# Optimization experiments

Hardware: AMD Instinct MI355X
Metric: run time of the kernel (lower is better)

## Reference

```python
import jax, jax.numpy as jnp
import numpy as np

B, S, D, H = 4, 2048, 1024, 16
HD = D // H


def setup_inputs() -> dict:
    key = jax.random.key(0)
    ks = jax.random.split(key, 12)
    sc = 0.02
    inp = {
        "q": jax.random.normal(ks[0], (B, S, D), jnp.float32),
        "k": jax.random.normal(ks[1], (B, S, D), jnp.float32),
        "v": jax.random.normal(ks[2], (B, S, D), jnp.float32),
        "mask": jnp.tril(jnp.ones((S, S), jnp.int32))[None, None],  # causal [1,1,S,S]
        "Wq": jax.random.normal(ks[3], (D, D), jnp.float32) * sc,
        "bq": jnp.zeros((D,), jnp.float32),
        "Wk": jax.random.normal(ks[4], (D, D), jnp.float32) * sc,
        "bk": jnp.zeros((D,), jnp.float32),
        "Wv": jax.random.normal(ks[5], (D, D), jnp.float32) * sc,
        "bv": jnp.zeros((D,), jnp.float32),
        "Wo": jax.random.normal(ks[6], (D, D), jnp.float32) * sc,
        "bo": jnp.zeros((D,), jnp.float32),
    }
    return inp


def reference(q, k, v, mask, Wq, bq, Wk, bk, Wv, bv, Wo, bo):
    # Linear projections (torch Linear: x @ W.T + b)
    qh = (q @ Wq.T + bq).reshape(B, S, H, HD).transpose(0, 2, 1, 3)  # [B,H,S,hd]
    kh = (k @ Wk.T + bk).reshape(B, S, H, HD).transpose(0, 2, 1, 3)
    vh = (v @ Wv.T + bv).reshape(B, S, H, HD).transpose(0, 2, 1, 3)
    score = jnp.einsum("bhqd,bhkd->bhqk", qh, kh) / jnp.sqrt(jnp.float32(HD))
    score = jnp.where(mask == 0, jnp.float32(-10000.0), score)
    attn = jax.nn.softmax(score, axis=-1)
    out = jnp.einsum("bhqk,bhkd->bhqd", attn, vh)  # [B,H,S,hd]
    out = out.transpose(0, 2, 1, 3).reshape(B, S, D)
    return out @ Wo.T + bo
```

## Files before the change

### kernel.cpp

```cpp
#include <hip/hip_runtime.h>

#define S_LEN 2048
#define D_DIM 1024
#define NB    4
#define NH    16
#define HDIM  64
#define PLD   72
#define QSCL  0.18033688011112042f

typedef float  f32x4  __attribute__((ext_vector_type(4)));
typedef __bf16 bf16x4 __attribute__((ext_vector_type(4)));
typedef __bf16 bf16x8 __attribute__((ext_vector_type(8)));

static __device__ __forceinline__ f32x4 mfma16(bf16x8 a, bf16x8 b, f32x4 c) {
  return __builtin_amdgcn_mfma_f32_16x16x32_bf16(a, b, c, 0, 0, 0);
}
static __device__ __forceinline__ bf16x4 cvt4(f32x4 v) {
  return __builtin_convertvector(v, bf16x4);
}
static __device__ __forceinline__ bf16x8 cvt8(f32x4 lo, f32x4 hi) {
  bf16x4 a = cvt4(lo), b = cvt4(hi);
  bf16x8 r;
  r[0] = a[0]; r[1] = a[1]; r[2] = a[2]; r[3] = a[3];
  r[4] = b[0]; r[5] = b[1]; r[6] = b[2]; r[7] = b[3];
  return r;
}
static __device__ __forceinline__ void cp16(const void* g, void* l) {
  __builtin_amdgcn_global_load_lds(
      (const __attribute__((address_space(1))) unsigned int*)g,
      (__attribute__((address_space(3))) unsigned int*)l, 16, 0, 0);
}

__global__ __launch_bounds__(256) void conv_w(
    const float* __restrict__ Wq, const float* __restrict__ Wk,
    const float* __restrict__ Wv, const float* __restrict__ Wo,
    __bf16* __restrict__ out)
{
  const float* src;
  if (blockIdx.y == 0) src = Wq;
  else if (blockIdx.y == 1) src = Wk;
  else if (blockIdx.y == 2) src = Wv;
  else src = Wo;
  size_t i = ((size_t)blockIdx.x * 256 + threadIdx.x) * 4;
  f32x4 v = *(const f32x4*)(src + i);
  *(bf16x4*)(out + (size_t)blockIdx.y * (D_DIM * D_DIM) + i) = cvt4(v);
}

__global__ __launch_bounds__(256) void conv_a(
    const float* __restrict__ q, const float* __restrict__ k,
    const float* __restrict__ v, __bf16* __restrict__ out)
{
  const float* src;
  if (blockIdx.y == 0) src = q;
  else if (blockIdx.y == 1) src = k;
  else src = v;
  size_t i = ((size_t)blockIdx.x * 256 + threadIdx.x) * 4;
  f32x4 x = *(const f32x4*)(src + i);
  *(bf16x4*)(out + (size_t)blockIdx.y * ((size_t)NB * S_LEN * D_DIM) + i) = cvt4(x);
}

static __device__ __forceinline__ void proj_epilogue(
    f32x4 (&acc)[4][4], int z, int mbase, int nbase, int wm, int wn,
    int l15, int quad, const float* bias,
    __bf16* qh, __bf16* kh, __bf16* vt)
{
  const float scl = (z == 0) ? QSCL : 1.0f;
#pragma unroll
  for (int mt = 0; mt < 4; ++mt)
#pragma unroll
    for (int nt = 0; nt < 4; ++nt) {
      int n = nbase + wn + nt * 16 + l15;
      int h = n >> 6, hd = n & 63;
      float bb = bias[n];
      f32x4 vv = acc[mt][nt];
#pragma unroll
      for (int r = 0; r < 4; ++r) vv[r] = (vv[r] + bb) * scl;
      bf16x4 pv = cvt4(vv);
      int m0 = mbase + wm + mt * 16 + quad * 4;
      int b = m0 >> 11, s0 = m0 & 2047;
      if (z == 2) {
        *(bf16x4*)(vt + ((size_t)((b * NH + h) * HDIM + hd)) * S_LEN + s0) = pv;
      } else {
        __bf16* out = (z == 0) ? qh : kh;
#pragma unroll
        for (int r = 0; r < 4; ++r)
          out[((size_t)(b * NH + h) * S_LEN + s0 + r) * HDIM + hd] = pv[r];
      }
    }
}

__global__ __launch_bounds__(256, 4) void proj_bf16(
    const __bf16* __restrict__ abf, const __bf16* __restrict__ Wbf,
    const float* __restrict__ bq, const float* __restrict__ bk, const float* __restrict__ bv,
    __bf16* __restrict__ qh, __bf16* __restrict__ kh, __bf16* __restrict__ vt)
{
  const __bf16* A = abf + (size_t)blockIdx.z * ((size_t)NB * S_LEN * D_DIM);
  const __bf16* W = Wbf + (size_t)blockIdx.z * (D_DIM * D_DIM);
  const float* bias = (blockIdx.z == 0) ? bq : (blockIdx.z == 1) ? bk : bv;

  __shared__ __bf16 As[128 * 64];
  __shared__ __bf16 Bs[128 * 64];

  const int tid  = threadIdx.x;
  const int wave = tid >> 6;
  const int lane = tid & 63;
  const int l15  = lane & 15;
  const int quad = lane >> 4;
  const int mbase = blockIdx.x * 128;
  const int nbase = blockIdx.y * 128;
  const int wm = (wave & 1) * 64;
  const int wn = (wave >> 1) * 64;
  const int brow = lane >> 3;
  const int scol = ((lane & 7) ^ (brow & 7)) * 8;
  const int swz  = l15 & 7;

  f32x4 acc[4][4] = {};

  for (int kt = 0; kt < D_DIM; kt += 64) {
#pragma unroll
    for (int c = 0; c < 4; ++c) {
      int r = wave * 32 + c * 8 + brow;
      cp16(A + (size_t)(mbase + r) * D_DIM + kt + scol, As + r * 64);
      cp16(W + (size_t)(nbase + r) * D_DIM + kt + scol, Bs + r * 64);
    }
    __syncthreads();

#pragma unroll
    for (int k0 = 0; k0 < 2; ++k0) {
      bf16x8 af[4], bfr[4];
#pragma unroll
      for (int i = 0; i < 4; ++i) {
        int off = ((k0 * 4 + quad) ^ swz) * 8;
        af[i]  = *(const bf16x8*)(As + (wm + i * 16 + l15) * 64 + off);
        bfr[i] = *(const bf16x8*)(Bs + (wn + i * 16 + l15) * 64 + off);
      }
#pragma unroll
      for (int mt = 0; mt < 4; ++mt)
#pragma unroll
        for (int nt = 0; nt < 4; ++nt)
          acc[mt][nt] = mfma16(af[mt], bfr[nt], acc[mt][nt]);
    }
    __syncthreads();
  }

  proj_epilogue(acc, blockIdx.z, mbase, nbase, wm, wn, l15, quad, bias, qh, kh, vt);
}

__global__ __launch_bounds__(256, 2) void proj_f32(
    const float* __restrict__ qin, const float* __restrict__ kin, const float* __restrict__ vin,
    const __bf16* __restrict__ Wbf,
    const float* __restrict__ bq, const float* __restrict__ bk, const float* __restrict__ bv,
    __bf16* __restrict__ qh, __bf16* __restrict__ kh, __bf16* __restrict__ vt)
{
  const float* A; const float* bias;
  if (blockIdx.z == 0)      { A = qin; bias = bq; }
  else if (blockIdx.z == 1) { A = kin; bias = bk; }
  else                      { A = vin; bias = bv; }
  const __bf16* W = Wbf + (size_t)blockIdx.z * (D_DIM * D_DIM);

  __shared__ float  As[128 * 64];
  __shared__ __bf16 Bs[128 * 64];

  const int tid  = threadIdx.x;
  const int wave = tid >> 6;
  const int lane = tid & 63;
  const int l15  = lane & 15;
  const int quad = lane >> 4;
  const int mbase = blockIdx.x * 128;
  const int nbase = blockIdx.y * 128;
  const int wm = (wave & 1) * 64;
  const int wn = (wave >> 1) * 64;
  const int arow = lane >> 4;
  const int brow = lane >> 3;

  f32x4 acc[4][4] = {};

  for (int kt = 0; kt < D_DIM; kt += 64) {
#pragma unroll
    for (int c = 0; c < 8; ++c) {
      int rr = c * 4 + arow;
      int r  = wave * 32 + rr;
      int col = ((lane & 15) ^ (rr & 15)) * 4;
      cp16(A + (size_t)(mbase + r) * D_DIM + kt + col, As + r * 64);
    }
#pragma unroll
    for (int c = 0; c < 4; ++c) {
      int r  = wave * 32 + c * 8 + brow;
      int col = ((lane & 7) ^ (brow & 7)) * 8;
      cp16(W + (size_t)(nbase + r) * D_DIM + kt + col, Bs + r * 64);
    }
    __syncthreads();

#pragma unroll
    for (int k0 = 0; k0 < 2; ++k0) {
      bf16x8 af[4], bfr[4];
#pragma unroll
      for (int i = 0; i < 4; ++i) {
        const float* ap = As + (wm + i * 16 + l15) * 64;
        int c0 = k0 * 8 + quad * 2;
        f32x4 lo = *(const f32x4*)(ap + ((c0 ^ l15) * 4));
        f32x4 hi = *(const f32x4*)(ap + (((c0 + 1) ^ l15) * 4));
        af[i] = cvt8(lo, hi);
        bfr[i] = *(const bf16x8*)(Bs + (wn + i * 16 + l15) * 64 +
                                  (((k0 * 4 + quad) ^ (l15 & 7)) * 8));
      }
#pragma unroll
      for (int mt = 0; mt < 4; ++mt)
#pragma unroll
        for (int nt = 0; nt < 4; ++nt)
          acc[mt][nt] = mfma16(af[mt], bfr[nt], acc[mt][nt]);
    }
    __syncthreads();
  }

  proj_epilogue(acc, blockIdx.z, mbase, nbase, wm, wn, l15, quad, bias, qh, kh, vt);
}

__global__ __launch_bounds__(256, 4) void attn_kernel(
    const __bf16* __restrict__ qh, const __bf16* __restrict__ kh,
    const __bf16* __restrict__ vt, __bf16* __restrict__ ao)
{
  __shared__ __bf16 Kb[64 * 64];
  __shared__ __bf16 Vb[64 * 64];
  __shared__ __bf16 Ps[4][16 * PLD];

  const int bh = blockIdx.y;
  const int x  = blockIdx.x;
  const __bf16* qp = qh + (size_t)bh * S_LEN * HDIM;
  const __bf16* kp = kh + (size_t)bh * S_LEN * HDIM;
  const __bf16* vp = vt + (size_t)bh * HDIM * S_LEN;

  const int tid  = threadIdx.x;
  const int wave = tid >> 6;
  const int lane = tid & 63;
  const int l15  = lane & 15;
  const int quad = lane >> 4;
  const int w16  = wave * 16;
  const int srow = lane >> 3;
  const int scol = ((lane & 7) ^ srow) * 8;
  const int swz  = l15 & 7;
  const int b = bh >> 4, h = bh & 15;

  __bf16* wps = &Ps[wave][0];

  for (int ph = 0; ph < 2; ++ph) {
    const int qc = ph ? (31 - x) : x;
    const int qb = qc * 64;

    bf16x8 fq[2];
    {
      const __bf16* qrow = qp + (size_t)(qb + w16 + l15) * HDIM;
      fq[0] = *(const bf16x8*)(qrow + quad * 8);
      fq[1] = *(const bf16x8*)(qrow + 32 + quad * 8);
    }
    f32x4 accO[4] = {};
    float l_run[4] = {0.f, 0.f, 0.f, 0.f};

    for (int kt = 0; kt <= qc; ++kt) {
      __syncthreads();
#pragma unroll
      for (int c = 0; c < 2; ++c) {
        int rb = w16 + c * 8;
        cp16(kp + (size_t)(kt * 64 + rb + srow) * HDIM + scol,  &Kb[rb * 64]);
        cp16(vp + (size_t)(rb + srow) * S_LEN + kt * 64 + scol, &Vb[rb * 64]);
      }
      __syncthreads();

      f32x4 sc[4] = {};
#pragma unroll
      for (int k0 = 0; k0 < 2; ++k0)
#pragma unroll
        for (int nt = 0; nt < 4; ++nt) {
          bf16x8 bk = *(const bf16x8*)(Kb + (nt * 16 + l15) * 64 + (((k0 * 4 + quad) ^ swz) * 8));
          sc[nt] = mfma16(fq[k0], bk, sc[nt]);
        }

      const bool diag = (kt == qc);
#pragma unroll
      for (int nt = 0; nt < 4; ++nt) {
        f32x4 p;
#pragma unroll
        for (int r = 0; r < 4; ++r) {
          float pv = exp2f(sc[nt][r]);
          if (diag && (nt * 16 + l15 > w16 + quad * 4 + r)) pv = 0.f;
          l_run[r] += pv;
          p[r] = pv;
        }
        bf16x4 pb = cvt4(p);
#pragma unroll
        for (int r = 0; r < 4; ++r)
          wps[(quad * 4 + r) * PLD + nt * 16 + l15] = pb[r];
      }

#pragma unroll
      for (int k0 = 0; k0 < 2; ++k0) {
        bf16x8 ap = *(const bf16x8*)(wps + l15 * PLD + k0 * 32 + quad * 8);
#pragma unroll
        for (int nt = 0; nt < 4; ++nt) {
          bf16x8 bv = *(const bf16x8*)(Vb + (nt * 16 + l15) * 64 + (((k0 * 4 + quad) ^ swz) * 8));
          accO[nt] = mfma16(ap, bv, accO[nt]);
        }
      }
    }

#pragma unroll
    for (int r = 0; r < 4; ++r) {
      float s = l_run[r];
      s += __shfl_xor(s, 1); s += __shfl_xor(s, 2);
      s += __shfl_xor(s, 4); s += __shfl_xor(s, 8);
      l_run[r] = s;
    }
#pragma unroll
    for (int nt = 0; nt < 4; ++nt) {
      f32x4 ov;
#pragma unroll
      for (int r = 0; r < 4; ++r) ov[r] = accO[nt][r] / l_run[r];
      bf16x4 ob = cvt4(ov);
#pragma unroll
      for (int r = 0; r < 4; ++r) {
        int sr = qb + w16 + quad * 4 + r;
        ao[((size_t)b * S_LEN + sr) * D_DIM + h * HDIM + nt * 16 + l15] = ob[r];
      }
    }
  }
}

__global__ __launch_bounds__(256, 4) void out_gemm(
    const __bf16* __restrict__ Ain, const __bf16* __restrict__ Wbf,
    const float* __restrict__ bo, float* __restrict__ Cout)
{
  __shared__ __bf16 As[128 * 64];
  __shared__ __bf16 Bs[128 * 64];

  const int tid  = threadIdx.x;
  const int wave = tid >> 6;
  const int lane = tid & 63;
  const int l15  = lane & 15;
  const int quad = lane >> 4;
  const int mbase = blockIdx.x * 128;
  const int nbase = blockIdx.y * 128;
  const int wm = (wave & 1) * 64;
  const int wn = (wave >> 1) * 64;
  const int brow = lane >> 3;
  const int scol = ((lane & 7) ^ (brow & 7)) * 8;
  const int swz  = l15 & 7;

  f32x4 acc[4][4] = {};

  for (int kt = 0; kt < D_DIM; kt += 64) {
#pragma unroll
    for (int c = 0; c < 4; ++c) {
      int r = wave * 32 + c * 8 + brow;
      cp16(Ain + (size_t)(mbase + r) * D_DIM + kt + scol, As + r * 64);
      cp16(Wbf + (size_t)(nbase + r) * D_DIM + kt + scol, Bs + r * 64);
    }
    __syncthreads();

#pragma unroll
    for (int k0 = 0; k0 < 2; ++k0) {
      bf16x8 af[4], bfr[4];
#pragma unroll
      for (int i = 0; i < 4; ++i) {
        int off = ((k0 * 4 + quad) ^ swz) * 8;
        af[i]  = *(const bf16x8*)(As + (wm + i * 16 + l15) * 64 + off);
        bfr[i] = *(const bf16x8*)(Bs + (wn + i * 16 + l15) * 64 + off);
      }
#pragma unroll
      for (int mt = 0; mt < 4; ++mt)
#pragma unroll
        for (int nt = 0; nt < 4; ++nt)
          acc[mt][nt] = mfma16(af[mt], bfr[nt], acc[mt][nt]);
    }
    __syncthreads();
  }

#pragma unroll
  for (int mt = 0; mt < 4; ++mt)
#pragma unroll
    for (int nt = 0; nt < 4; ++nt) {
      int n = nbase + wn + nt * 16 + l15;
      float bb = bo[n];
      int m0 = mbase + wm + mt * 16 + quad * 4;
#pragma unroll
      for (int r = 0; r < 4; ++r)
        Cout[(size_t)(m0 + r) * D_DIM + n] = acc[mt][nt][r] + bb;
    }
}

extern "C" void kernel_launch(void* const* d_in, const int* in_sizes, int n_in,
                              void* d_out, int out_size, void* d_ws, size_t ws_size,
                              hipStream_t stream) {
  const float* q  = (const float*)d_in[0];
  const float* k  = (const float*)d_in[1];
  const float* v  = (const float*)d_in[2];
  const float* Wq = (const float*)d_in[4];
  const float* bq = (const float*)d_in[5];
  const float* Wk = (const float*)d_in[6];
  const float* bk = (const float*)d_in[7];
  const float* Wv = (const float*)d_in[8];
  const float* bv = (const float*)d_in[9];
  const float* Wo = (const float*)d_in[10];
  const float* bo = (const float*)d_in[11];

  __bf16* ws = (__bf16*)d_ws;
  const size_t WSZ = (size_t)D_DIM * D_DIM;
  const size_t NE  = (size_t)NB * S_LEN * D_DIM;
  __bf16* wbf = ws;
  __bf16* qh  = ws + 4 * WSZ;
  __bf16* kh  = qh + NE;
  __bf16* vt  = kh + NE;
  __bf16* ao  = vt + NE;
  __bf16* abf = vt + NE;
  const size_t NEED = (size_t)(4 * WSZ + 3 * NE + 3 * NE) * sizeof(__bf16);

  const bool useBf16A = (ws_size >= NEED);

  conv_w<<<dim3(1024, 4), 256, 0, stream>>>(Wq, Wk, Wv, Wo, wbf);
  if (useBf16A) {
    conv_a<<<dim3(8192, 3), 256, 0, stream>>>(q, k, v, abf);
    proj_bf16<<<dim3(64, 8, 3), 256, 0, stream>>>(abf, wbf, bq, bk, bv, qh, kh, vt);
  } else {
    proj_f32<<<dim3(64, 8, 3), 256, 0, stream>>>(q, k, v, wbf, bq, bk, bv, qh, kh, vt);
  }
  attn_kernel<<<dim3(16, 64), 256, 0, stream>>>(qh, kh, vt, ao);
  out_gemm<<<dim3(64, 8), 256, 0, stream>>>(ao, wbf + 3 * WSZ, bo, (float*)d_out);
}
```

Before: 339.1 us.

## Fuse both causal query chunks into one K/V sweep in attention

The attention kernel no longer runs its two balanced query chunks (x and 31-x) one after the other. It runs them together in a single loop over K/V tiles, so each K/V tile loaded into shared memory serves both chunks while the smaller chunk is still active. The QK^T MFMA now takes its operands in swapped order, which lets P be written as vector bf16x4 stores and makes the row-sum reduction cheaper. It also switches to the raw exp2 builtin and multiplies by a reciprocal instead of dividing. The costs are more registers for two sets of accumulators, which may hurt occupancy, and per-tile branching on whether the first chunk is still active.

After: 315.1 us. 1.08x faster.

```diff
diff --git a/kernel.cpp b/kernel.cpp
--- a/kernel.cpp
+++ b/kernel.cpp
@@ -222,10 +222,11 @@
 {
   __shared__ __bf16 Kb[64 * 64];
   __shared__ __bf16 Vb[64 * 64];
-  __shared__ __bf16 Ps[4][16 * PLD];
+  __shared__ __bf16 Ps[4][2][16 * PLD];
 
   const int bh = blockIdx.y;
   const int x  = blockIdx.x;
+  const int qc0 = x, qc1 = 31 - x;
   const __bf16* qp = qh + (size_t)bh * S_LEN * HDIM;
   const __bf16* kp = kh + (size_t)bh * S_LEN * HDIM;
   const __bf16* vp = vt + (size_t)bh * HDIM * S_LEN;
@@ -241,81 +242,109 @@
   const int swz  = l15 & 7;
   const int b = bh >> 4, h = bh & 15;
 
-  __bf16* wps = &Ps[wave][0];
-
-  for (int ph = 0; ph < 2; ++ph) {
-    const int qc = ph ? (31 - x) : x;
-    const int qb = qc * 64;
-
-    bf16x8 fq[2];
-    {
-      const __bf16* qrow = qp + (size_t)(qb + w16 + l15) * HDIM;
-      fq[0] = *(const bf16x8*)(qrow + quad * 8);
-      fq[1] = *(const bf16x8*)(qrow + 32 + quad * 8);
-    }
-    f32x4 accO[4] = {};
-    float l_run[4] = {0.f, 0.f, 0.f, 0.f};
-
-    for (int kt = 0; kt <= qc; ++kt) {
-      __syncthreads();
-#pragma unroll
-      for (int c = 0; c < 2; ++c) {
-        int rb = w16 + c * 8;
-        cp16(kp + (size_t)(kt * 64 + rb + srow) * HDIM + scol,  &Kb[rb * 64]);
-        cp16(vp + (size_t)(rb + srow) * S_LEN + kt * 64 + scol, &Vb[rb * 64]);
-      }
-      __syncthreads();
-
-      f32x4 sc[4] = {};
-#pragma unroll
-      for (int k0 = 0; k0 < 2; ++k0)
+  bf16x8 fq[2][2];
+#pragma unroll
+  for (int j = 0; j < 2; ++j) {
+    const int qb = (j ? qc1 : qc0) * 64;
+    const __bf16* qrow = qp + (size_t)(qb + w16 + l15) * HDIM;
+    fq[j][0] = *(const bf16x8*)(qrow + quad * 8);
+    fq[j][1] = *(const bf16x8*)(qrow + 32 + quad * 8);
+  }
+
+  f32x4 accO[2][4] = {};
+  float lp[2] = {0.f, 0.f};
+
+  for (int kt = 0; kt <= qc1; ++kt) {
+    __syncthreads();
+#pragma unroll
+    for (int c = 0; c < 2; ++c) {
+      int rb = w16 + c * 8;
+      cp16(kp + (size_t)(kt * 64 + rb + srow) * HDIM + scol,  &Kb[rb * 64]);
+      cp16(vp + (size_t)(rb + srow) * S_LEN + kt * 64 + scol, &Vb[rb * 64]);
+    }
+    __syncthreads();
+
+    const bool act0 = (kt <= qc0);
+
+    f32x4 sc[2][4] = {};
+#pragma unroll
+    for (int k0 = 0; k0 < 2; ++k0)
+#pragma unroll
+      for (int nt = 0; nt < 4; ++nt) {
+        bf16x8 bk = *(const bf16x8*)(Kb + (nt * 16 + l15) * 64 + (((k0 * 4 + quad) ^ swz) * 8));
+        if (act0) sc[0][nt] = mfma16(bk, fq[0][k0], sc[0][nt]);
+        sc[1][nt] = mfma16(bk, fq[1][k0], sc[1][nt]);
+      }
+
+#pragma unroll
+    for (int j = 0; j < 2; ++j) {
+      if (j == 0 && !act0) continue;
+      const int qcj = j ? qc1 : qc0;
+      __bf16* wp = &Ps[wave][j][0];
+      float ls = 0.f;
+      if (kt == qcj) {
 #pragma unroll
         for (int nt = 0; nt < 4; ++nt) {
-          bf16x8 bk = *(const bf16x8*)(Kb + (nt * 16 + l15) * 64 + (((k0 * 4 + quad) ^ swz) * 8));
-          sc[nt] = mfma16(fq[k0], bk, sc[nt]);
+          f32x4 p;
+#pragma unroll
+          for (int r = 0; r < 4; ++r) {
+            float pv = __builtin_amdgcn_exp2f(sc[j][nt][r]);
+            if (nt * 16 + quad * 4 + r > w16 + l15) pv = 0.f;
+            ls += pv;
+            p[r] = pv;
+          }
+          *(bf16x4*)(wp + l15 * PLD + nt * 16 + quad * 4) = cvt4(p);
         }
-
-      const bool diag = (kt == qc);
+      } else {
+#pragma unroll
+        for (int nt = 0; nt < 4; ++nt) {
+          f32x4 p;
+#pragma unroll
+          for (int r = 0; r < 4; ++r) {
+            float pv = __builtin_amdgcn_exp2f(sc[j][nt][r]);
+            ls += pv;
+            p[r] = pv;
+          }
+          *(bf16x4*)(wp + l15 * PLD + nt * 16 + quad * 4) = cvt4(p);
+        }
+      }
+      lp[j] += ls;
+    }
+
+#pragma unroll
+    for (int k0 = 0; k0 < 2; ++k0) {
+      bf16x8 ap0, ap1;
+      if (act0) ap0 = *(const bf16x8*)(&Ps[wave][0][0] + l15 * PLD + k0 * 32 + quad * 8);
+      ap1 = *(const bf16x8*)(&Ps[wave][1][0] + l15 * PLD + k0 * 32 + quad * 8);
 #pragma unroll
       for (int nt = 0; nt < 4; ++nt) {
-        f32x4 p;
-#pragma unroll
-        for (int r = 0; r < 4; ++r) {
-          float pv = exp2f(sc[nt][r]);
-          if (diag && (nt * 16 + l15 > w16 + quad * 4 + r)) pv = 0.f;
-          l_run[r] += pv;
-          p[r] = pv;
-        }
-        bf16x4 pb = cvt4(p);
-#pragma unroll
-        for (int r = 0; r < 4; ++r)
-          wps[(quad * 4 + r) * PLD + nt * 16 + l15] = pb[r];
-      }
-
-#pragma unroll
-      for (int k0 = 0; k0 < 2; ++k0) {
-        bf16x8 ap = *(const bf16x8*)(wps + l15 * PLD + k0 * 32 + quad * 8);
-#pragma unroll
-        for (int nt = 0; nt < 4; ++nt) {
-          bf16x8 bv = *(const bf16x8*)(Vb + (nt * 16 + l15) * 64 + (((k0 * 4 + quad) ^ swz) * 8));
-          accO[nt] = mfma16(ap, bv, accO[nt]);
-        }
-      }
-    }
-
+        bf16x8 bv = *(const bf16x8*)(Vb + (nt * 16 + l15) * 64 + (((k0 * 4 + quad) ^ swz) * 8));
+        if (act0) accO[0][nt] = mfma16(ap0, bv, accO[0][nt]);
+        accO[1][nt] = mfma16(ap1, bv, accO[1][nt]);
+      }
+    }
+  }
+
+#pragma unroll
+  for (int j = 0; j < 2; ++j) {
+    float lf = lp[j];
+    lf += __shfl_xor(lf, 16);
+    lf += __shfl_xor(lf, 32);
+    const int qb = (j ? qc1 : qc0) * 64;
 #pragma unroll
     for (int r = 0; r < 4; ++r) {
-      float s = l_run[r];
-      s += __shfl_xor(s, 1); s += __shfl_xor(s, 2);
-      s += __shfl_xor(s, 4); s += __shfl_xor(s, 8);
-      l_run[r] = s;
+      float inv = 1.0f / __shfl(lf, quad * 4 + r);
+      f32x4 dummy;
+      (void)dummy;
+#pragma unroll
+      for (int nt = 0; nt < 4; ++nt) {
+      }
+#pragma unroll
+      for (int nt = 0; nt < 4; ++nt) accO[j][nt][r] *= inv;
     }
 #pragma unroll
     for (int nt = 0; nt < 4; ++nt) {
-      f32x4 ov;
-#pragma unroll
-      for (int r = 0; r < 4; ++r) ov[r] = accO[nt][r] / l_run[r];
-      bf16x4 ob = cvt4(ov);
+      bf16x4 ob = cvt4(accO[j][nt]);
 #pragma unroll
       for (int r = 0; r < 4; ++r) {
         int sr = qb + w16 + quad * 4 + r;
@@ -411,7 +440,7 @@
   __bf16* vt  = kh + NE;
   __bf16* ao  = vt + NE;
   __bf16* abf = vt + NE;
-  const size_t NEED = (size_t)(4 * WSZ + 3 * NE + 3 * NE) * sizeof(__bf16);
+  const size_t NEED = (size_t)(4 * WSZ + 6 * NE) * sizeof(__bf16);
 
   const bool useBf16A = (ws_size >= NEED);
 
```
